# Kernel tuning notes

Measured on AMD Instinct MI355X. Metric: run time of the kernel, lower is better.

The kernel has to match this reference:

```python
import jax, jax.numpy as jnp
import numpy as np

RES = (16, 16, 16)          # grid resolution per example
FEAT_DIM = 8                # channels stored per grid vertex
NUM_EMB = 2048
HID = (64, 64)
OUT_DIM = 16
B, N = 64, 8192             # nexmp, npnts


def setup_inputs() -> dict:
    key = jax.random.key(0)
    ks = jax.random.split(key, 9)
    ttl = FEAT_DIM * int(np.prod(RES))
    idx = jax.random.randint(ks[0], (B,), 0, NUM_EMB)
    x = jax.random.uniform(ks[1], (B, N, 3), jnp.float32, -0.5, 0.5)
    emb = jax.random.normal(ks[2], (NUM_EMB, ttl), jnp.float32) * 0.02
    W0 = jax.random.normal(ks[3], (FEAT_DIM, HID[0]), jnp.float32) / np.sqrt(FEAT_DIM).astype(np.float32)
    b0 = jnp.zeros((HID[0],), jnp.float32)
    W1 = jax.random.normal(ks[4], (HID[0], HID[1]), jnp.float32) / np.sqrt(HID[0]).astype(np.float32)
    b1 = jnp.zeros((HID[1],), jnp.float32)
    Wout = jax.random.normal(ks[5], (HID[1], OUT_DIM), jnp.float32) / np.sqrt(HID[1]).astype(np.float32)
    bout = jnp.zeros((OUT_DIM,), jnp.float32)
    return {"idx": idx, "x": x, "emb": emb, "W0": W0, "b0": b0,
            "W1": W1, "b1": b1, "Wout": Wout, "bout": bout}


def trilinear_resample(grid, locs):
    """grid: [B, D, H, W, C]; locs: [B, N, 3] in (x, y, z) order (xyz coord order,
    x indexes the last spatial axis). CONSTANT_OUTSIDE: out-of-range corners -> 0."""
    Bn = grid.shape[0]
    D, H, W = grid.shape[1:4]
    f = jnp.floor(locs)
    t = locs - f                      # fractional part, [B, N, 3]
    f = f.astype(jnp.int32)
    bidx = jnp.arange(Bn)[:, None]    # [B, 1] broadcast over points
    out = jnp.zeros(locs.shape[:-1] + (grid.shape[-1],), grid.dtype)
    for dz in (0, 1):
        for dy in (0, 1):
            for dx in (0, 1):
                ix = f[..., 0] + dx
                iy = f[..., 1] + dy
                iz = f[..., 2] + dz
                w = ((t[..., 0] if dx else 1.0 - t[..., 0])
                     * (t[..., 1] if dy else 1.0 - t[..., 1])
                     * (t[..., 2] if dz else 1.0 - t[..., 2]))
                valid = ((ix >= 0) & (ix < W) & (iy >= 0) & (iy < H)
                         & (iz >= 0) & (iz < D))
                v = grid[bidx,
                         jnp.clip(iz, 0, D - 1),
                         jnp.clip(iy, 0, H - 1),
                         jnp.clip(ix, 0, W - 1)]          # [B, N, C]
                out = out + (w * valid.astype(grid.dtype))[..., None] * v
    return out


def reference(idx, x, emb, W0, b0, W1, b1, Wout, bout):
    nexmp, npnts, _ = x.shape
    # per-example grid gathered from the embedding table
    grid = emb[idx].reshape((nexmp,) + RES + (FEAT_DIM,))   # [B, D, H, W, C]
    res_arr = jnp.asarray(RES, x.dtype)
    locs = (x + 0.5) * (res_arr - 1.0)                      # [B, N, 3]
    feat = trilinear_resample(grid, locs)                   # [B, N, C]
    h = jax.nn.leaky_relu(feat @ W0 + b0, negative_slope=0.01)
    h = jax.nn.leaky_relu(h @ W1 + b1, negative_slope=0.01)
    return h @ Wout + bout                                  # [B, N, OUT_DIM]
```

## Files before the change

### kernel.cpp

```cpp
#include <hip/hip_runtime.h>


typedef __attribute__((ext_vector_type(8)))  short short8;
typedef __attribute__((ext_vector_type(16))) float f32x16;
typedef __attribute__((ext_vector_type(4)))  int   int4v;

static __device__ __forceinline__ unsigned cvt_pk_bf16(float lo, float hi) {
    unsigned r;
    asm("v_cvt_pk_bf16_f32 %0, %1, %2" : "=v"(r) : "v"(lo), "v"(hi));
    return r;
}
static __device__ __forceinline__ void permswap(unsigned &a, unsigned &b) {
    asm("v_permlane32_swap_b32 %0, %1" : "+v"(a), "+v"(b));
}
static __device__ __forceinline__ short8 as_s8(int4v v) {
    return __builtin_bit_cast(short8, v);
}

static __device__ __forceinline__ void relu_pack_ct(f32x16 acc[2], int4v bfr[4]) {
    #pragma unroll
    for (int rt = 0; rt < 2; ++rt)
        #pragma unroll
        for (int r = 0; r < 16; ++r) {
            float a = acc[rt][r];
            acc[rt][r] = fmaxf(a, 0.01f * a);
        }
    #pragma unroll
    for (int kt = 0; kt < 4; ++kt) {
        const int rs = kt >> 1;
        const int base = (kt & 1) * 8;
        unsigned pa0 = cvt_pk_bf16(acc[rs][base + 0], acc[rs][base + 1]);
        unsigned pa1 = cvt_pk_bf16(acc[rs][base + 2], acc[rs][base + 3]);
        unsigned pb0 = cvt_pk_bf16(acc[rs][base + 4], acc[rs][base + 5]);
        unsigned pb1 = cvt_pk_bf16(acc[rs][base + 6], acc[rs][base + 7]);
        permswap(pa0, pb0);
        permswap(pa1, pb1);
        bfr[kt][0] = (int)pa0;
        bfr[kt][1] = (int)pa1;
        bfr[kt][2] = (int)pb0;
        bfr[kt][3] = (int)pb1;
    }
}

__global__ __launch_bounds__(512) void featmlp_mfma(
    const int* __restrict__ idx,
    const float* __restrict__ x,
    const float* __restrict__ emb,
    const float* __restrict__ W0, const float* __restrict__ b0,
    const float* __restrict__ W1, const float* __restrict__ b1,
    const float* __restrict__ Wout, const float* __restrict__ bout,
    float* __restrict__ out)
{
    __shared__ int4v frag_lds[17 * 64];

    const int tid  = threadIdx.x;
    const int warp = tid >> 6;
    const int lane = tid & 63;
    const int half = lane >> 5;
    const int l31  = lane & 31;

    const int bid = blockIdx.x;
    const int swz = (bid & 7) * 128 + (bid >> 3);
    const int group = swz * 8 + warp;
    const long pbase = (long)group * 64;
    const int  b  = group >> 7;

    const float* __restrict__ g = emb + ((long)idx[b] << 15);

    const long p = pbase + lane;
    const float x0 = x[p * 3 + 0];
    const float x1 = x[p * 3 + 1];
    const float x2 = x[p * 3 + 2];

    const float lx = (x0 + 0.5f) * 15.0f;
    const float ly = (x1 + 0.5f) * 15.0f;
    const float lz = (x2 + 0.5f) * 15.0f;
    const float fx = floorf(lx), fy = floorf(ly), fz = floorf(lz);
    const float wx1 = lx - fx, wy1 = ly - fy, wz1 = lz - fz;
    const float wx0 = 1.0f - wx1, wy0 = 1.0f - wy1, wz0 = 1.0f - wz1;
    const int ix = (int)fx, iy = (int)fy, iz = (int)fz;
    const int vbase = ((iz * 16) + iy) * 16 + ix;

    float feat[8];
    #pragma unroll
    for (int c = 0; c < 8; ++c) feat[c] = 0.0f;
    #pragma unroll
    for (int dz = 0; dz < 2; ++dz) {
        const float wz = dz ? wz1 : wz0;
        #pragma unroll
        for (int dy = 0; dy < 2; ++dy) {
            const float wzy = wz * (dy ? wy1 : wy0);
            #pragma unroll
            for (int dx = 0; dx < 2; ++dx) {
                const float w = wzy * (dx ? wx1 : wx0);
                const float4* v = (const float4*)(g + (long)(vbase + dz * 256 + dy * 16 + dx) * 8);
                const float4 v0 = v[0];
                const float4 v1 = v[1];
                feat[0] += w * v0.x; feat[1] += w * v0.y;
                feat[2] += w * v0.z; feat[3] += w * v0.w;
                feat[4] += w * v1.x; feat[5] += w * v1.y;
                feat[6] += w * v1.z; feat[7] += w * v1.w;
            }
        }
    }

    int4v bf0[2];
    #pragma unroll
    for (int m = 0; m < 4; ++m) {
        unsigned a = cvt_pk_bf16(feat[2 * m], feat[2 * m + 1]);
        unsigned z = (m == 0) ? 0x00003f80u : 0u;
        permswap(a, z);
        bf0[0][m] = (int)a;
        bf0[1][m] = (int)z;
    }

    for (int fid = warp; fid < 17; fid += 8) {
        int4v f;
        if (fid < 2) {
            const int j = fid * 32 + l31;
            if (half == 0) {
                #pragma unroll
                for (int m = 0; m < 4; ++m)
                    f[m] = (int)cvt_pk_bf16(W0[(2 * m) * 64 + j], W0[(2 * m + 1) * 64 + j]);
            } else {
                f[0] = (int)cvt_pk_bf16(b0[j], 0.0f);
                f[1] = 0; f[2] = 0; f[3] = 0;
            }
        } else if (fid < 12) {
            const int t = fid - 2;
            const int rt = t / 5, kt = t % 5;
            const int j = rt * 32 + l31;
            if (kt < 4) {
                #pragma unroll
                for (int m = 0; m < 4; ++m) {
                    const int k = kt * 16 + half * 8 + 2 * m;
                    f[m] = (int)cvt_pk_bf16(W1[k * 64 + j], W1[(k + 1) * 64 + j]);
                }
            } else {
                f[0] = half ? 0 : (int)cvt_pk_bf16(b1[j], 0.0f);
                f[1] = 0; f[2] = 0; f[3] = 0;
            }
        } else {
            const int kt = fid - 12;
            const int jo = l31 < 15 ? l31 : 15;
            if (kt < 4) {
                #pragma unroll
                for (int m = 0; m < 4; ++m) {
                    const int k = kt * 16 + half * 8 + 2 * m;
                    f[m] = (int)cvt_pk_bf16(Wout[k * 16 + jo], Wout[(k + 1) * 16 + jo]);
                }
            } else {
                f[0] = half ? 0 : (int)cvt_pk_bf16(bout[jo], 0.0f);
                f[1] = 0; f[2] = 0; f[3] = 0;
            }
        }
        frag_lds[fid * 64 + lane] = f;
    }

    __syncthreads();

    int4v b1x;
    b1x[0] = half ? 0 : 0x00003f80;
    b1x[1] = 0; b1x[2] = 0; b1x[3] = 0;

    f32x16 zc;
    #pragma unroll
    for (int i = 0; i < 16; ++i) zc[i] = 0.0f;

    #pragma unroll
    for (int ct = 0; ct < 2; ++ct) {
        f32x16 acc0[2];
        #pragma unroll
        for (int rt = 0; rt < 2; ++rt) {
            const int4v wf = frag_lds[rt * 64 + lane];
            acc0[rt] = __builtin_amdgcn_mfma_f32_32x32x16_bf16(
                as_s8(wf), as_s8(bf0[ct]), zc, 0, 0, 0);
        }

        int4v b1f[4];
        relu_pack_ct(acc0, b1f);

        f32x16 acc1[2];
        #pragma unroll
        for (int rt = 0; rt < 2; ++rt) {
            f32x16 a = zc;
            #pragma unroll
            for (int kt = 0; kt < 4; ++kt) {
                const int4v wf = frag_lds[(2 + rt * 5 + kt) * 64 + lane];
                a = __builtin_amdgcn_mfma_f32_32x32x16_bf16(
                    as_s8(wf), as_s8(b1f[kt]), a, 0, 0, 0);
            }
            const int4v wb = frag_lds[(2 + rt * 5 + 4) * 64 + lane];
            acc1[rt] = __builtin_amdgcn_mfma_f32_32x32x16_bf16(
                as_s8(wb), as_s8(b1x), a, 0, 0, 0);
        }

        int4v b2f[4];
        relu_pack_ct(acc1, b2f);

        f32x16 a = zc;
        #pragma unroll
        for (int kt = 0; kt < 4; ++kt) {
            const int4v wf = frag_lds[(12 + kt) * 64 + lane];
            a = __builtin_amdgcn_mfma_f32_32x32x16_bf16(
                as_s8(wf), as_s8(b2f[kt]), a, 0, 0, 0);
        }
        const int4v wb = frag_lds[16 * 64 + lane];
        a = __builtin_amdgcn_mfma_f32_32x32x16_bf16(
            as_s8(wb), as_s8(b1x), a, 0, 0, 0);

        float* o = out + (pbase + ct * 32 + l31) * 16;
        *(float4*)(o + half * 4)     = make_float4(a[0], a[1], a[2], a[3]);
        *(float4*)(o + 8 + half * 4) = make_float4(a[4], a[5], a[6], a[7]);
    }
}

extern "C" void kernel_launch(void* const* d_in, const int* in_sizes, int n_in,
                              void* d_out, int out_size, void* d_ws, size_t ws_size,
                              hipStream_t stream) {
    const int*   idx  = (const int*)  d_in[0];
    const float* x    = (const float*)d_in[1];
    const float* emb  = (const float*)d_in[2];
    const float* W0   = (const float*)d_in[3];
    const float* b0   = (const float*)d_in[4];
    const float* W1   = (const float*)d_in[5];
    const float* b1   = (const float*)d_in[6];
    const float* Wout = (const float*)d_in[7];
    const float* bout = (const float*)d_in[8];
    float* out = (float*)d_out;

    featmlp_mfma<<<1024, 512, 0, stream>>>(idx, x, emb, W0, b0, W1, b1,
                                           Wout, bout, out);
}
```

Before: 30.31 us.

## Split trilinear interpolation into separate kernel writing bf16 features to workspace

Adds a standalone interpolation kernel (256-thread blocks) that gathers the trilinear features and writes them as packed bf16 to the workspace. The MLP kernel then only reads 16 bytes per point, so its MFMA part no longer waits on the latency-bound grid gathers. When no workspace is available, a fused fallback runs instead, with the gather moved after the weight-fragment staging. The split adds a second launch plus an 8 MB write and read round trip through global memory.

Result: slower. 36.73 us (+21.2%).

```diff
diff --git a/kernel.cpp b/kernel.cpp
--- a/kernel.cpp
+++ b/kernel.cpp
@@ -15,6 +15,63 @@
 }
 static __device__ __forceinline__ short8 as_s8(int4v v) {
     return __builtin_bit_cast(short8, v);
+}
+
+__global__ __launch_bounds__(256) void interp_kernel(
+    const int* __restrict__ idx,
+    const float* __restrict__ x,
+    const float* __restrict__ emb,
+    int4v* __restrict__ ws)
+{
+    const int bid = blockIdx.x;
+    const int swz = (bid & 7) * 256 + (bid >> 3);
+    const long p = (long)swz * 256 + threadIdx.x;
+    const int  b = swz >> 5;
+
+    const float* __restrict__ g = emb + ((long)idx[b] << 15);
+
+    const float x0 = x[p * 3 + 0];
+    const float x1 = x[p * 3 + 1];
+    const float x2 = x[p * 3 + 2];
+
+    const float lx = (x0 + 0.5f) * 15.0f;
+    const float ly = (x1 + 0.5f) * 15.0f;
+    const float lz = (x2 + 0.5f) * 15.0f;
+    const float fx = floorf(lx), fy = floorf(ly), fz = floorf(lz);
+    const float wx1 = lx - fx, wy1 = ly - fy, wz1 = lz - fz;
+    const float wx0 = 1.0f - wx1, wy0 = 1.0f - wy1, wz0 = 1.0f - wz1;
+    const int ix = (int)fx, iy = (int)fy, iz = (int)fz;
+    const int vbase = ((iz * 16) + iy) * 16 + ix;
+
+    float feat[8];
+    #pragma unroll
+    for (int c = 0; c < 8; ++c) feat[c] = 0.0f;
+    #pragma unroll
+    for (int dz = 0; dz < 2; ++dz) {
+        const float wz = dz ? wz1 : wz0;
+        #pragma unroll
+        for (int dy = 0; dy < 2; ++dy) {
+            const float wzy = wz * (dy ? wy1 : wy0);
+            #pragma unroll
+            for (int dx = 0; dx < 2; ++dx) {
+                const float w = wzy * (dx ? wx1 : wx0);
+                const float4* v = (const float4*)(g + (long)(vbase + dz * 256 + dy * 16 + dx) * 8);
+                const float4 v0 = v[0];
+                const float4 v1 = v[1];
+                feat[0] += w * v0.x; feat[1] += w * v0.y;
+                feat[2] += w * v0.z; feat[3] += w * v0.w;
+                feat[4] += w * v1.x; feat[5] += w * v1.y;
+                feat[6] += w * v1.z; feat[7] += w * v1.w;
+            }
+        }
+    }
+
+    int4v f;
+    f[0] = (int)cvt_pk_bf16(feat[0], feat[1]);
+    f[1] = (int)cvt_pk_bf16(feat[2], feat[3]);
+    f[2] = (int)cvt_pk_bf16(feat[4], feat[5]);
+    f[3] = (int)cvt_pk_bf16(feat[6], feat[7]);
+    ws[p] = f;
 }
 
 static __device__ __forceinline__ void relu_pack_ct(f32x16 acc[2], int4v bfr[4]) {
@@ -42,13 +99,16 @@
     }
 }
 
-__global__ __launch_bounds__(512) void featmlp_mfma(
+
+template <bool FUSED>
+__global__ __launch_bounds__(512) void mlp_kernel(
     const int* __restrict__ idx,
     const float* __restrict__ x,
     const float* __restrict__ emb,
     const float* __restrict__ W0, const float* __restrict__ b0,
     const float* __restrict__ W1, const float* __restrict__ b1,
     const float* __restrict__ Wout, const float* __restrict__ bout,
+    const int4v* __restrict__ ws,
     float* __restrict__ out)
 {
     __shared__ int4v frag_lds[17 * 64];
@@ -65,53 +125,14 @@
     const long pbase = (long)group * 64;
     const int  b  = group >> 7;
 
+    int4v fv;
+    float x0, x1, x2;
     const float* __restrict__ g = emb + ((long)idx[b] << 15);
-
     const long p = pbase + lane;
-    const float x0 = x[p * 3 + 0];
-    const float x1 = x[p * 3 + 1];
-    const float x2 = x[p * 3 + 2];
-
-    const float lx = (x0 + 0.5f) * 15.0f;
-    const float ly = (x1 + 0.5f) * 15.0f;
-    const float lz = (x2 + 0.5f) * 15.0f;
-    const float fx = floorf(lx), fy = floorf(ly), fz = floorf(lz);
-    const float wx1 = lx - fx, wy1 = ly - fy, wz1 = lz - fz;
-    const float wx0 = 1.0f - wx1, wy0 = 1.0f - wy1, wz0 = 1.0f - wz1;
-    const int ix = (int)fx, iy = (int)fy, iz = (int)fz;
-    const int vbase = ((iz * 16) + iy) * 16 + ix;
-
-    float feat[8];
-    #pragma unroll
-    for (int c = 0; c < 8; ++c) feat[c] = 0.0f;
-    #pragma unroll
-    for (int dz = 0; dz < 2; ++dz) {
-        const float wz = dz ? wz1 : wz0;
-        #pragma unroll
-        for (int dy = 0; dy < 2; ++dy) {
-            const float wzy = wz * (dy ? wy1 : wy0);
-            #pragma unroll
-            for (int dx = 0; dx < 2; ++dx) {
-                const float w = wzy * (dx ? wx1 : wx0);
-                const float4* v = (const float4*)(g + (long)(vbase + dz * 256 + dy * 16 + dx) * 8);
-                const float4 v0 = v[0];
-                const float4 v1 = v[1];
-                feat[0] += w * v0.x; feat[1] += w * v0.y;
-                feat[2] += w * v0.z; feat[3] += w * v0.w;
-                feat[4] += w * v1.x; feat[5] += w * v1.y;
-                feat[6] += w * v1.z; feat[7] += w * v1.w;
-            }
-        }
-    }
-
-    int4v bf0[2];
-    #pragma unroll
-    for (int m = 0; m < 4; ++m) {
-        unsigned a = cvt_pk_bf16(feat[2 * m], feat[2 * m + 1]);
-        unsigned z = (m == 0) ? 0x00003f80u : 0u;
-        permswap(a, z);
-        bf0[0][m] = (int)a;
-        bf0[1][m] = (int)z;
+    if (FUSED) {
+        x0 = x[p * 3 + 0]; x1 = x[p * 3 + 1]; x2 = x[p * 3 + 2];
+    } else {
+        fv = ws[p];
     }
 
     for (int fid = warp; fid < 17; fid += 8) {
@@ -157,7 +178,55 @@
         frag_lds[fid * 64 + lane] = f;
     }
 
+    if (FUSED) {
+        const float lx = (x0 + 0.5f) * 15.0f;
+        const float ly = (x1 + 0.5f) * 15.0f;
+        const float lz = (x2 + 0.5f) * 15.0f;
+        const float fx = floorf(lx), fy = floorf(ly), fz = floorf(lz);
+        const float wx1 = lx - fx, wy1 = ly - fy, wz1 = lz - fz;
+        const float wx0 = 1.0f - wx1, wy0 = 1.0f - wy1, wz0 = 1.0f - wz1;
+        const int ix = (int)fx, iy = (int)fy, iz = (int)fz;
+        const int vbase = ((iz * 16) + iy) * 16 + ix;
+
+        float feat[8];
+        #pragma unroll
+        for (int c = 0; c < 8; ++c) feat[c] = 0.0f;
+        #pragma unroll
+        for (int dz = 0; dz < 2; ++dz) {
+            const float wz = dz ? wz1 : wz0;
+            #pragma unroll
+            for (int dy = 0; dy < 2; ++dy) {
+                const float wzy = wz * (dy ? wy1 : wy0);
+                #pragma unroll
+                for (int dx = 0; dx < 2; ++dx) {
+                    const float w = wzy * (dx ? wx1 : wx0);
+                    const float4* v = (const float4*)(g + (long)(vbase + dz * 256 + dy * 16 + dx) * 8);
+                    const float4 v0 = v[0];
+                    const float4 v1 = v[1];
+                    feat[0] += w * v0.x; feat[1] += w * v0.y;
+                    feat[2] += w * v0.z; feat[3] += w * v0.w;
+                    feat[4] += w * v1.x; feat[5] += w * v1.y;
+                    feat[6] += w * v1.z; feat[7] += w * v1.w;
+                }
+            }
+        }
+        fv[0] = (int)cvt_pk_bf16(feat[0], feat[1]);
+        fv[1] = (int)cvt_pk_bf16(feat[2], feat[3]);
+        fv[2] = (int)cvt_pk_bf16(feat[4], feat[5]);
+        fv[3] = (int)cvt_pk_bf16(feat[6], feat[7]);
+    }
+
     __syncthreads();
+
+    int4v bf0[2];
+    #pragma unroll
+    for (int m = 0; m < 4; ++m) {
+        unsigned a = (unsigned)fv[m];
+        unsigned z = (m == 0) ? 0x00003f80u : 0u;
+        permswap(a, z);
+        bf0[0][m] = (int)a;
+        bf0[1][m] = (int)z;
+    }
 
     int4v b1x;
     b1x[0] = half ? 0 : 0x00003f80;
@@ -229,6 +298,14 @@
     const float* bout = (const float*)d_in[8];
     float* out = (float*)d_out;
 
-    featmlp_mfma<<<1024, 512, 0, stream>>>(idx, x, emb, W0, b0, W1, b1,
-                                           Wout, bout, out);
-}
+    const size_t need = 524288ull * 16;
+    if (ws_size >= need && d_ws != nullptr) {
+        int4v* ws = (int4v*)d_ws;
+        interp_kernel<<<2048, 256, 0, stream>>>(idx, x, emb, ws);
+        mlp_kernel<false><<<1024, 512, 0, stream>>>(idx, x, emb, W0, b0, W1, b1,
+                                                    Wout, bout, ws, out);
+    } else {
+        mlp_kernel<true><<<1024, 512, 0, stream>>>(idx, x, emb, W0, b0, W1, b1,
+                                                   Wout, bout, (const int4v*)nullptr, out);
+    }
+}
```
